# Performance work log

Hardware: AMD Instinct MI355X
Metric: run time of the kernel (lower is better)

## Reference

```python
import jax, jax.numpy as jnp
import numpy as np

LATENT = 256
C = 512            # channels == window_size
STEP = C // 2      # 256
N_SAMPLES = 32768
N_FRAMES = N_SAMPLES // STEP   # 128
IMP = 4096         # impulse samples
B, E = 4, 64
EPS = 1e-8


def unit_norm(x, axis=-1):
    return x / (jnp.linalg.norm(x, axis=axis, keepdims=True) + EPS)


def hamming(n):
    # torch.hamming_window default (periodic=True)
    return (0.54 - 0.46 * jnp.cos(2.0 * jnp.pi * jnp.arange(n) / n)).astype(jnp.float32)


def layer_norm(x, g, b):
    mu = x.mean(-1, keepdims=True)
    var = x.var(-1, keepdims=True)
    return (x - mu) / jnp.sqrt(var + 1e-5) * g + b


def mlp(x, Ws, bs, g, bt):
    # LinearOutputStack: 3 hidden (linear -> LayerNorm -> leaky_relu) + output linear
    for j in range(3):
        x = x @ Ws[j] + bs[j]
        x = layer_norm(x, g[j], bt[j])
        x = jax.nn.leaky_relu(x, 0.2)
    return x @ Ws[3] + bs[3]


def _forward(embedding, impulse, W_def, b_def,
             Ws_imp, bs_imp, g_imp, bt_imp,
             Ws_lat, bs_lat, g_lat, bt_lat,
             Ws_out, bs_out, g_out, bt_out,
             W_w, b_w, W_b, b_b, W_l, b_l):
    Bq, Eq, _ = embedding.shape
    # shape deformations: latent -> (C, n_frames), unit-normed over channel dim
    deform = (embedding @ W_def + b_def).reshape(Bq, Eq, C, N_FRAMES)
    deform = unit_norm(deform, axis=2)
    deform = deform.transpose(0, 1, 3, 2)           # (B,E,T,C)
    weights = deform @ W_w + b_w                    # (B,E,T,C)
    biases = deform @ W_b + b_b                     # (B,E,T,C)
    leak = 0.1 + jax.nn.sigmoid(deform @ W_l + b_l) * 0.98  # (B,E,T,1)

    # window the impulse: frames of size C with hop STEP
    padded = jnp.pad(impulse, ((0, 0), (0, 0), (0, STEP)))
    starts = jnp.arange(IMP // STEP) * STEP
    idx = starts[:, None] + jnp.arange(C)[None, :]
    windowed = padded[..., idx]                     # (B,E,16,C)
    norms = jnp.linalg.norm(windowed, axis=-1, keepdims=True)
    emb = mlp(windowed, Ws_imp, bs_imp, g_imp, bt_imp)
    emb = unit_norm(emb) * norms                    # (B,E,16,C)
    # pad with zeros to n_frames: adding zero == original i < n_impulse_frames guard
    emb_pad = jnp.pad(emb, ((0, 0), (0, 0), (0, N_FRAMES - emb.shape[2]), (0, 0)))

    ham = hamming(C)

    xs = (weights.transpose(2, 0, 1, 3),
          biases.transpose(2, 0, 1, 3),
          leak.transpose(2, 0, 1, 3),
          emb_pad.transpose(2, 0, 1, 3))

    def step(h, x):
        w, b, lk, e = x
        h = h + e
        cn = jnp.linalg.norm(h, axis=-1, keepdims=True)
        h = h * w + b
        h = unit_norm(h) * cn
        ol = mlp(h, Ws_lat, bs_lat, g_lat, bt_lat)
        ol = unit_norm(ol) * (cn * lk)
        on = jnp.linalg.norm(ol, axis=-1, keepdims=True)
        h = h - ol
        h = unit_norm(h) * (cn - on)
        of = mlp(ol, Ws_out, bs_out, g_out, bt_out)
        of = of * ham
        of = unit_norm(of) * on
        return h, of

    h0 = jnp.zeros((Bq, Eq, C), dtype=embedding.dtype)
    _, frames = jax.lax.scan(step, h0, xs)          # (T,B,E,C)
    frames = frames.transpose(1, 2, 0, 3)           # (B,E,T,C)

    # overlap-add at hop STEP, trim to n_samples
    L = (N_FRAMES - 1) * STEP + C
    oa_idx = jnp.arange(N_FRAMES)[:, None] * STEP + jnp.arange(C)[None, :]
    out = jnp.zeros((Bq, Eq, L), dtype=embedding.dtype)
    out = out.at[:, :, oa_idx].add(frames)
    return out[..., :N_SAMPLES]


def setup_inputs() -> dict:
    key = jax.random.key(0)
    ks = jax.random.split(key, 24)
    s = 0.02
    d = {
        'embedding': jax.random.normal(ks[0], (B, E, LATENT), jnp.float32),
        'impulse': jax.random.normal(ks[1], (B, E, IMP), jnp.float32),
        'W_def': jax.random.normal(ks[2], (LATENT, C * N_FRAMES), jnp.float32) * s,
        'b_def': jnp.zeros((C * N_FRAMES,), jnp.float32),
        'W_w': jax.random.normal(ks[3], (C, C), jnp.float32) * s,
        'b_w': jnp.zeros((C,), jnp.float32),
        'W_b': jax.random.normal(ks[4], (C, C), jnp.float32) * s,
        'b_b': jnp.zeros((C,), jnp.float32),
        'W_l': jax.random.normal(ks[5], (C, 1), jnp.float32) * s,
        'b_l': jnp.zeros((1,), jnp.float32),
    }
    for name, k in (('imp', ks[6]), ('lat', ks[7]), ('out', ks[8])):
        d['Ws_' + name] = jax.random.normal(k, (4, C, C), jnp.float32) * s
        d['bs_' + name] = jnp.zeros((4, C), jnp.float32)
        d['g_' + name] = jnp.ones((3, C), jnp.float32)
        d['bt_' + name] = jnp.zeros((3, C), jnp.float32)
    return d


def reference(embedding, impulse, W_def, b_def,
              Ws_imp, bs_imp, g_imp, bt_imp,
              Ws_lat, bs_lat, g_lat, bt_lat,
              Ws_out, bs_out, g_out, bt_out,
              W_w, b_w, W_b, b_b, W_l, b_l):
    return _forward(embedding, impulse, W_def, b_def,
                    Ws_imp, bs_imp, g_imp, bt_imp,
                    Ws_lat, bs_lat, g_lat, bt_lat,
                    Ws_out, bs_out, g_out, bt_out,
                    W_w, b_w, W_b, b_b, W_l, b_l)
```

## Files before the change

### kernel.cpp

```cpp
#include <hip/hip_runtime.h>
#include <math.h>

#define NB 4
#define NE 64
#define BE 256
#define LAT 256
#define NC 512
#define NT 128
#define NDEF 65536
#define NIMP 4096
#define NF 16
#define EPSN 1e-8f
#define SPB 4
#define NSCAN 64

typedef unsigned short ushort8 __attribute__((ext_vector_type(8)));
typedef short short8v __attribute__((ext_vector_type(8)));
typedef float f32x4 __attribute__((ext_vector_type(4)));

__device__ __forceinline__ unsigned short f2bf(float f) {
  const unsigned u = __float_as_uint(f);
  return (unsigned short)((u + 0x7FFFu + ((u >> 16) & 1u)) >> 16);
}

__device__ __forceinline__ void bar_nodrain() {
  asm volatile("s_waitcnt lgkmcnt(0)" ::: "memory");
  __builtin_amdgcn_s_barrier();
  __builtin_amdgcn_sched_barrier(0);
}

template <int NR>
__device__ __forceinline__ void blk_reduce1(const float* v, float* out,
                                            float* red) {
  const int tid = threadIdx.x, wave = tid >> 6, lane = tid & 63;
  float s[NR];
#pragma unroll
  for (int i = 0; i < NR; ++i) s[i] = v[i];
#pragma unroll
  for (int off = 32; off; off >>= 1) {
#pragma unroll
    for (int i = 0; i < NR; ++i) s[i] += __shfl_down(s[i], off);
  }
  if (lane == 0) {
#pragma unroll
    for (int i = 0; i < NR; ++i) red[wave * NR + i] = s[i];
  }
  bar_nodrain();
#pragma unroll
  for (int i = 0; i < NR; ++i) {
    float a = 0.f;
#pragma unroll
    for (int w = 0; w < 8; ++w) a += red[w * NR + i];
    out[i] = a;
  }
}

__global__ __launch_bounds__(64) void k_cvt(const float* __restrict__ W,
                                            unsigned short* __restrict__ Wmf) {
  const int lane = threadIdx.x;
  const int gg = blockIdx.x;
  const int p = gg & 3;
  const int kt = (gg >> 2) & 15;
  const int wv = (gg >> 6) & 7;
  const int layer = gg >> 9;
  const int col = wv * 64 + p * 16 + (lane & 15);
  const int k0 = kt * 32 + (lane >> 4) * 8;
  ushort8 o;
#pragma unroll
  for (int j = 0; j < 8; ++j)
    o[j] = f2bf(W[((size_t)layer * NC + k0 + j) * NC + col]);
  *reinterpret_cast<ushort8*>(Wmf + ((size_t)gg * 64 + lane) * 8) = o;
}

__global__ __launch_bounds__(256) void k_deform(
    const float* __restrict__ emb, const float* __restrict__ Wd,
    const float* __restrict__ bd, float* __restrict__ deform) {
  __shared__ float As[32][LAT];
  const int tid = threadIdx.x;
  const int c = blockIdx.x * 256 + tid;
  const int m0 = blockIdx.y * 32;
  for (int i = 0; i < 32; ++i) As[i][tid] = emb[(m0 + i) * LAT + tid];
  __syncthreads();
  float acc[32];
#pragma unroll
  for (int i = 0; i < 32; ++i) acc[i] = 0.f;
  for (int k = 0; k < LAT; k += 4) {
    const float w0 = Wd[(size_t)(k + 0) * NDEF + c];
    const float w1 = Wd[(size_t)(k + 1) * NDEF + c];
    const float w2 = Wd[(size_t)(k + 2) * NDEF + c];
    const float w3 = Wd[(size_t)(k + 3) * NDEF + c];
#pragma unroll
    for (int i = 0; i < 32; ++i) {
      const float4 a = *reinterpret_cast<const float4*>(&As[i][k]);
      acc[i] = fmaf(a.x, w0, acc[i]);
      acc[i] = fmaf(a.y, w1, acc[i]);
      acc[i] = fmaf(a.z, w2, acc[i]);
      acc[i] = fmaf(a.w, w3, acc[i]);
    }
  }
  const float bv = bd[c];
  for (int i = 0; i < 32; ++i)
    deform[(size_t)(m0 + i) * NDEF + c] = acc[i] + bv;
}

__global__ __launch_bounds__(512) void k_wb(
    const float* __restrict__ deform, const float* __restrict__ Ww,
    const float* __restrict__ bw, const float* __restrict__ Wb,
    const float* __restrict__ bb, const float* __restrict__ Wl,
    const float* __restrict__ bl, float* __restrict__ weights,
    float* __restrict__ biases, float* __restrict__ leak) {
  __shared__ float xs[16][NC];
  __shared__ float rno[16], lks[16];
  const int tid = threadIdx.x;
  const int wave = tid >> 6, lane = tid & 63;
  const int be = blockIdx.x >> 3;
  const int t0 = (blockIdx.x & 7) * 16;
  const float* dbase = deform + (size_t)be * NDEF;
  for (int i = 0; i < 16; ++i)
    xs[i][tid] = dbase[(size_t)tid * NT + t0 + i];
  __syncthreads();
  for (int f = wave; f < 16; f += 8) {
    float s = 0.f;
#pragma unroll
    for (int j = 0; j < 8; ++j) {
      const float v = xs[f][lane + 64 * j];
      s = fmaf(v, v, s);
    }
#pragma unroll
    for (int off = 32; off; off >>= 1) s += __shfl_down(s, off);
    if (lane == 0) rno[f] = sqrtf(s);
  }
  __syncthreads();
#pragma unroll
  for (int i = 0; i < 16; ++i) xs[i][tid] = xs[i][tid] / (rno[i] + EPSN);
  __syncthreads();
  for (int f = wave; f < 16; f += 8) {
    float s = 0.f;
#pragma unroll
    for (int j = 0; j < 8; ++j)
      s = fmaf(xs[f][lane + 64 * j], Wl[lane + 64 * j], s);
#pragma unroll
    for (int off = 32; off; off >>= 1) s += __shfl_down(s, off);
    if (lane == 0) lks[f] = s;
  }
  __syncthreads();
  if (tid < 16) {
    const float v = lks[tid] + bl[0];
    leak[(size_t)be * NT + t0 + tid] = 0.1f + 0.98f / (1.f + expf(-v));
  }
  float accw[16], accb[16];
#pragma unroll
  for (int i = 0; i < 16; ++i) { accw[i] = 0.f; accb[i] = 0.f; }
  for (int k = 0; k < NC; k += 2) {
    const float w0 = Ww[(size_t)k * NC + tid];
    const float w1 = Ww[(size_t)(k + 1) * NC + tid];
    const float v0 = Wb[(size_t)k * NC + tid];
    const float v1 = Wb[(size_t)(k + 1) * NC + tid];
#pragma unroll
    for (int i = 0; i < 16; ++i) {
      const float2 a = *reinterpret_cast<const float2*>(&xs[i][k]);
      accw[i] = fmaf(a.x, w0, accw[i]);
      accw[i] = fmaf(a.y, w1, accw[i]);
      accb[i] = fmaf(a.x, v0, accb[i]);
      accb[i] = fmaf(a.y, v1, accb[i]);
    }
  }
  const float bwv = bw[tid], bbv = bb[tid];
  for (int i = 0; i < 16; ++i) {
    const size_t o = ((size_t)be * NT + t0 + i) * NC + tid;
    weights[o] = accw[i] + bwv;
    biases[o] = accb[i] + bbv;
  }
}

__device__ __forceinline__ void tile_gemm16(const float (*xs)[NC],
                                            const float* __restrict__ W,
                                            int tid, float acc[16]) {
#pragma unroll
  for (int i = 0; i < 16; ++i) acc[i] = 0.f;
  for (int k = 0; k < NC; k += 4) {
    const float w0 = W[(size_t)(k + 0) * NC + tid];
    const float w1 = W[(size_t)(k + 1) * NC + tid];
    const float w2 = W[(size_t)(k + 2) * NC + tid];
    const float w3 = W[(size_t)(k + 3) * NC + tid];
#pragma unroll
    for (int i = 0; i < 16; ++i) {
      const float4 a = *reinterpret_cast<const float4*>(&xs[i][k]);
      acc[i] = fmaf(a.x, w0, acc[i]);
      acc[i] = fmaf(a.y, w1, acc[i]);
      acc[i] = fmaf(a.z, w2, acc[i]);
      acc[i] = fmaf(a.w, w3, acc[i]);
    }
  }
}

__device__ __forceinline__ void ln_leaky16(float (*xs)[NC],
                                           const float* __restrict__ g,
                                           const float* __restrict__ bt,
                                           int layer, int tid, float* mu_s,
                                           float* rs_s) {
  const int wave = tid >> 6, lane = tid & 63;
  for (int f = wave; f < 16; f += 8) {
    float s = 0.f, s2 = 0.f;
#pragma unroll
    for (int j = 0; j < 8; ++j) {
      const float v = xs[f][lane + 64 * j];
      s += v;
      s2 = fmaf(v, v, s2);
    }
#pragma unroll
    for (int off = 32; off; off >>= 1) {
      s += __shfl_down(s, off);
      s2 += __shfl_down(s2, off);
    }
    if (lane == 0) {
      const float mu = s * (1.f / NC);
      mu_s[f] = mu;
      rs_s[f] = rsqrtf(s2 * (1.f / NC) - mu * mu + 1e-5f);
    }
  }
  __syncthreads();
  const float gv = g[layer * NC + tid], btv = bt[layer * NC + tid];
#pragma unroll
  for (int i = 0; i < 16; ++i) {
    const float y = (xs[i][tid] - mu_s[i]) * rs_s[i] * gv + btv;
    xs[i][tid] = y > 0.f ? y : 0.2f * y;
  }
  __syncthreads();
}

__global__ __launch_bounds__(512) void k_imp(
    const float* __restrict__ impulse, const float* __restrict__ Ws,
    const float* __restrict__ bs, const float* __restrict__ g,
    const float* __restrict__ bt, float* __restrict__ embo) {
  __shared__ float xs[16][NC];
  __shared__ float wno[16], mu_s[16], rs_s[16], ono[16];
  const int tid = threadIdx.x;
  const int wave = tid >> 6, lane = tid & 63;
  const int be = blockIdx.x;
  const float* ib = impulse + (size_t)be * NIMP;
  for (int f = 0; f < 16; ++f) {
    const int s = f * 256 + tid;
    xs[f][tid] = (s < NIMP) ? ib[s] : 0.f;
  }
  __syncthreads();
  for (int f = wave; f < 16; f += 8) {
    float s = 0.f;
#pragma unroll
    for (int j = 0; j < 8; ++j) {
      const float v = xs[f][lane + 64 * j];
      s = fmaf(v, v, s);
    }
#pragma unroll
    for (int off = 32; off; off >>= 1) s += __shfl_down(s, off);
    if (lane == 0) wno[f] = sqrtf(s);
  }
  __syncthreads();
  float acc[16];
  for (int layer = 0; layer < 4; ++layer) {
    tile_gemm16(xs, Ws + (size_t)layer * NC * NC, tid, acc);
    __syncthreads();
    const float bv = bs[layer * NC + tid];
#pragma unroll
    for (int i = 0; i < 16; ++i) xs[i][tid] = acc[i] + bv;
    __syncthreads();
    if (layer < 3) ln_leaky16(xs, g, bt, layer, tid, mu_s, rs_s);
  }
  for (int f = wave; f < 16; f += 8) {
    float s = 0.f;
#pragma unroll
    for (int j = 0; j < 8; ++j) {
      const float v = xs[f][lane + 64 * j];
      s = fmaf(v, v, s);
    }
#pragma unroll
    for (int off = 32; off; off >>= 1) s += __shfl_down(s, off);
    if (lane == 0) ono[f] = sqrtf(s);
  }
  __syncthreads();
  for (int f = 0; f < 16; ++f)
    embo[((size_t)be * NF + f) * NC + tid] =
        xs[f][tid] / (ono[f] + EPSN) * wno[f];
}

__global__ __launch_bounds__(512) void k_scan(
    const float* __restrict__ weights, const float* __restrict__ biases,
    const float* __restrict__ leak, const float* __restrict__ embw,
    const unsigned short* __restrict__ Wmf, const float* __restrict__ bs,
    const float* __restrict__ g, const float* __restrict__ bt,
    float* __restrict__ olb, float* __restrict__ onb) {
  __shared__ __align__(16) unsigned short A_lds[16 * NC];
  __shared__ __align__(16) unsigned short B_lds[8][4][2048];
  __shared__ float ol_lds[SPB][NC];
  __shared__ float redA[64];
  __shared__ float redB[32];
  __shared__ float st1[8][SPB], st2[8][SPB];
  __shared__ float lk_lds[SPB][NT];

  const int tid = threadIdx.x;
  const int wave = tid >> 6, lane = tid & 63;
  const int seq0 = blockIdx.x * SPB;

  {
    const int r = tid >> 7, tt = tid & 127;
    lk_lds[r][tt] = leak[(size_t)(seq0 + r) * NT + tt];
  }
  {
    unsigned* z = (unsigned*)(A_lds + SPB * NC);
    for (int i = tid; i < (16 - SPB) * NC / 2; i += 512) z[i] = 0u;
  }

  const int arow = lane & 15;
  const int kgrp = lane >> 4;
  const int abase = arow * (NC * 2);
  const int axor = (arow & 7) << 4;
  const int akoff = kgrp * 16;
  const bool crow = (kgrp == 0);

  float bsv[4][4], gv[3][4], btv[3][4];
#pragma unroll
  for (int p = 0; p < 4; ++p) {
    const int cp = wave * 64 + p * 16 + (lane & 15);
#pragma unroll
    for (int l = 0; l < 4; ++l) bsv[l][p] = bs[l * NC + cp];
#pragma unroll
    for (int l = 0; l < 3; ++l) {
      gv[l][p] = g[l * NC + cp];
      btv[l][p] = bt[l * NC + cp];
    }
  }
  const unsigned short* wfrag = Wmf + (size_t)wave * 32768 + lane * 8;

  auto issue_chunk = [&](int cc) {
    const int layer = cc >> 4, kt = cc & 15, slot = cc & 3;
#pragma unroll
    for (int p = 0; p < 4; ++p) {
      __builtin_amdgcn_global_load_lds(
          (const unsigned int*)(wfrag + (size_t)layer * 262144 +
                                (kt * 4 + p) * 512),
          (unsigned int*)&B_lds[wave][slot][p * 512], 16, 0, 0);
    }
  };

  float wpre[SPB], bpre[SPB], epre[SPB];
#pragma unroll
  for (int r = 0; r < SPB; ++r) {
    const size_t o = ((size_t)(seq0 + r) * NT) * NC + tid;
    wpre[r] = weights[o];
    bpre[r] = biases[o];
    epre[r] = embw[((size_t)(seq0 + r) * NF) * NC + tid];
  }

  __syncthreads();

  issue_chunk(0);
  issue_chunk(1);
  issue_chunk(2);

  float h[SPB], cn[SPB];
#pragma unroll
  for (int r = 0; r < SPB; ++r) { h[r] = 0.f; cn[r] = 0.f; }

#pragma unroll 1
  for (int t = 0; t < NT; ++t) {
    float hw[SPB];
    if (t < NF) {
#pragma unroll
      for (int r = 0; r < SPB; ++r) h[r] += epre[r];
      if (t + 1 < NF) {
#pragma unroll
        for (int r = 0; r < SPB; ++r)
          epre[r] = embw[((size_t)(seq0 + r) * NF + t + 1) * NC + tid];
      }
      float v8[8], s8[8];
#pragma unroll
      for (int r = 0; r < SPB; ++r) {
        hw[r] = fmaf(h[r], wpre[r], bpre[r]);
        v8[r] = h[r] * h[r];
        v8[SPB + r] = hw[r] * hw[r];
      }
      blk_reduce1<8>(v8, s8, redA);
#pragma unroll
      for (int r = 0; r < SPB; ++r) {
        cn[r] = sqrtf(s8[r]);
        h[r] = hw[r] * (cn[r] / (sqrtf(s8[SPB + r]) + EPSN));
      }
    } else {
      float v4[SPB], s4[SPB];
#pragma unroll
      for (int r = 0; r < SPB; ++r) {
        hw[r] = fmaf(h[r], wpre[r], bpre[r]);
        v4[r] = hw[r] * hw[r];
      }
      blk_reduce1<SPB>(v4, s4, redA);
#pragma unroll
      for (int r = 0; r < SPB; ++r)
        h[r] = hw[r] * (cn[r] / (sqrtf(s4[r]) + EPSN));
    }
    if (t + 1 < NT) {
#pragma unroll
      for (int r = 0; r < SPB; ++r) {
        const size_t o = ((size_t)(seq0 + r) * NT + t + 1) * NC + tid;
        wpre[r] = weights[o];
        bpre[r] = biases[o];
      }
    }
    {
      char* ab = (char*)A_lds;
#pragma unroll
      for (int r = 0; r < SPB; ++r)
        *(unsigned short*)(ab + r * 1024 + ((tid * 2) ^ ((r & 7) << 4))) =
            f2bf(h[r]);
    }
    bar_nodrain();

#pragma unroll 1
    for (int layer = 0; layer < 4; ++layer) {
      f32x4 acc[4];
#pragma unroll
      for (int p = 0; p < 4; ++p) acc[p] = (f32x4){0.f, 0.f, 0.f, 0.f};
#pragma unroll
      for (int kt = 0; kt < 16; ++kt) {
        asm volatile("s_waitcnt vmcnt(8)" ::: "memory");
        const short8v a = *(const short8v*)((const char*)A_lds + abase +
                                            (((kt * 64) + akoff) ^ axor));
        const int slot = kt & 3;
#pragma unroll
        for (int p = 0; p < 4; ++p) {
          const short8v b =
              *(const short8v*)((const char*)&B_lds[wave][slot][0] + p * 1024 +
                                lane * 16);
          acc[p] =
              __builtin_amdgcn_mfma_f32_16x16x32_bf16(a, b, acc[p], 0, 0, 0);
        }
        issue_chunk((layer * 16 + kt + 3) & 63);
      }

      if (layer < 3) {
        float s1[SPB], s2[SPB];
#pragma unroll
        for (int q = 0; q < SPB; ++q) { s1[q] = 0.f; s2[q] = 0.f; }
#pragma unroll
        for (int p = 0; p < 4; ++p) {
#pragma unroll
          for (int q = 0; q < SPB; ++q) {
            const float y = acc[p][q] + bsv[layer][p];
            acc[p][q] = y;
            s1[q] += y;
            s2[q] = fmaf(y, y, s2[q]);
          }
        }
#pragma unroll
        for (int off = 1; off < 16; off <<= 1) {
#pragma unroll
          for (int q = 0; q < SPB; ++q) {
            s1[q] += __shfl_xor(s1[q], off);
            s2[q] += __shfl_xor(s2[q], off);
          }
        }
        if (lane == 0) {
#pragma unroll
          for (int q = 0; q < SPB; ++q) {
            st1[wave][q] = s1[q];
            st2[wave][q] = s2[q];
          }
        }
        bar_nodrain();
        float mu[SPB], rs[SPB];
#pragma unroll
        for (int q = 0; q < SPB; ++q) {
          float a1 = 0.f, a2 = 0.f;
#pragma unroll
          for (int w = 0; w < 8; ++w) {
            a1 += st1[w][q];
            a2 += st2[w][q];
          }
          mu[q] = a1 * (1.f / NC);
          rs[q] = rsqrtf(a2 * (1.f / NC) - mu[q] * mu[q] + 1e-5f);
        }
        if (crow) {
          char* ab = (char*)A_lds;
#pragma unroll
          for (int q = 0; q < SPB; ++q) {
#pragma unroll
            for (int p = 0; p < 4; ++p) {
              float y = (acc[p][q] - mu[q]) * rs[q] * gv[layer][p] +
                        btv[layer][p];
              y = y > 0.f ? y : 0.2f * y;
              const int cp = wave * 64 + p * 16 + (lane & 15);
              *(unsigned short*)(ab + q * 1024 +
                                 ((cp * 2) ^ ((q & 7) << 4))) = f2bf(y);
            }
          }
        }
        bar_nodrain();
      } else {
        float s2[SPB];
#pragma unroll
        for (int q = 0; q < SPB; ++q) s2[q] = 0.f;
#pragma unroll
        for (int p = 0; p < 4; ++p) {
#pragma unroll
          for (int q = 0; q < SPB; ++q) {
            const float y = acc[p][q] + bsv[3][p];
            acc[p][q] = y;
            s2[q] = fmaf(y, y, s2[q]);
          }
        }
#pragma unroll
        for (int off = 1; off < 16; off <<= 1) {
#pragma unroll
          for (int q = 0; q < SPB; ++q) s2[q] += __shfl_xor(s2[q], off);
        }
        if (lane == 0) {
#pragma unroll
          for (int q = 0; q < SPB; ++q) st2[wave][q] = s2[q];
        }
        if (crow) {
#pragma unroll
          for (int q = 0; q < SPB; ++q) {
#pragma unroll
            for (int p = 0; p < 4; ++p)
              ol_lds[q][wave * 64 + p * 16 + (lane & 15)] = acc[p][q];
          }
        }
        bar_nodrain();
        float sc[SPB], on[SPB];
#pragma unroll
        for (int r = 0; r < SPB; ++r) {
          float a2 = 0.f;
#pragma unroll
          for (int w = 0; w < 8; ++w) a2 += st2[w][r];
          const float no = sqrtf(a2);
          sc[r] = cn[r] * lk_lds[r][t] / (no + EPSN);
          on[r] = no * sc[r];
        }
        if (tid < SPB) onb[(size_t)(seq0 + tid) * NT + t] = on[tid];
        float v4[SPB], s4[SPB];
#pragma unroll
        for (int r = 0; r < SPB; ++r) {
          const float olv = ol_lds[r][tid] * sc[r];
          olb[((size_t)(seq0 + r) * NT + t) * NC + tid] = olv;
          h[r] -= olv;
          v4[r] = h[r] * h[r];
        }
        blk_reduce1<SPB>(v4, s4, redB);
#pragma unroll
        for (int r = 0; r < SPB; ++r) {
          h[r] *= (cn[r] - on[r]) / (sqrtf(s4[r]) + EPSN);
          cn[r] = fabsf(cn[r] - on[r]);
        }
      }
    }
  }
}

__global__ __launch_bounds__(512) void k_out(
    const float* __restrict__ olb, const float* __restrict__ onb,
    const unsigned short* __restrict__ Wmf, const float* __restrict__ bs,
    const float* __restrict__ g, const float* __restrict__ bt,
    float* __restrict__ ofb) {
  __shared__ __align__(16) unsigned short A_lds[16 * NC];
  __shared__ float st1[8][16], st2[8][16];
  __shared__ float on_l[16];
  const int tid = threadIdx.x;
  const int wave = tid >> 6, lane = tid & 63;
  const int m0 = blockIdx.x * 16;
  const int arow = lane & 15;
  const int kgrp = lane >> 4;
  const int r0 = kgrp * 4;
  const int abase = arow * (NC * 2);
  const int axor = (arow & 7) << 4;
  const int akoff = kgrp * 16;

  float bsv[4][4], gv[3][4], btv[3][4], hamv[4];
#pragma unroll
  for (int p = 0; p < 4; ++p) {
    const int cp = wave * 64 + p * 16 + (lane & 15);
#pragma unroll
    for (int l = 0; l < 4; ++l) bsv[l][p] = bs[l * NC + cp];
#pragma unroll
    for (int l = 0; l < 3; ++l) {
      gv[l][p] = g[l * NC + cp];
      btv[l][p] = bt[l * NC + cp];
    }
    hamv[p] =
        0.54f - 0.46f * cosf(6.283185307179586f * (float)cp / (float)NC);
  }
  if (tid < 16) on_l[tid] = onb[m0 + tid];
  {
    char* ab = (char*)A_lds;
    for (int i = 0; i < 16; ++i) {
      const float v = olb[(size_t)(m0 + i) * NC + tid];
      *(unsigned short*)(ab + i * 1024 + ((tid * 2) ^ ((i & 7) << 4))) =
          f2bf(v);
    }
  }
  __syncthreads();

  const unsigned short* wfrag = Wmf + (size_t)wave * 32768 + lane * 8;

#pragma unroll 1
  for (int layer = 0; layer < 4; ++layer) {
    f32x4 acc[4];
#pragma unroll
    for (int p = 0; p < 4; ++p) acc[p] = (f32x4){0.f, 0.f, 0.f, 0.f};
#pragma unroll
    for (int kt = 0; kt < 16; ++kt) {
      const short8v a = *(const short8v*)((const char*)A_lds + abase +
                                          (((kt * 64) + akoff) ^ axor));
#pragma unroll
      for (int p = 0; p < 4; ++p) {
        const short8v b = *(const short8v*)(wfrag + (size_t)layer * 262144 +
                                            (kt * 4 + p) * 512);
        acc[p] = __builtin_amdgcn_mfma_f32_16x16x32_bf16(a, b, acc[p], 0, 0, 0);
      }
    }
    if (layer < 3) {
      float s1[4], s2[4];
#pragma unroll
      for (int q = 0; q < 4; ++q) { s1[q] = 0.f; s2[q] = 0.f; }
#pragma unroll
      for (int p = 0; p < 4; ++p) {
#pragma unroll
        for (int q = 0; q < 4; ++q) {
          const float y = acc[p][q] + bsv[layer][p];
          acc[p][q] = y;
          s1[q] += y;
          s2[q] = fmaf(y, y, s2[q]);
        }
      }
#pragma unroll
      for (int off = 1; off < 16; off <<= 1) {
#pragma unroll
        for (int q = 0; q < 4; ++q) {
          s1[q] += __shfl_xor(s1[q], off);
          s2[q] += __shfl_xor(s2[q], off);
        }
      }
      if ((lane & 15) == 0) {
#pragma unroll
        for (int q = 0; q < 4; ++q) {
          st1[wave][r0 + q] = s1[q];
          st2[wave][r0 + q] = s2[q];
        }
      }
      __syncthreads();
      char* ab = (char*)A_lds;
#pragma unroll
      for (int q = 0; q < 4; ++q) {
        const int row = r0 + q;
        float a1 = 0.f, a2 = 0.f;
#pragma unroll
        for (int w = 0; w < 8; ++w) {
          a1 += st1[w][row];
          a2 += st2[w][row];
        }
        const float mu = a1 * (1.f / NC);
        const float rs = rsqrtf(a2 * (1.f / NC) - mu * mu + 1e-5f);
#pragma unroll
        for (int p = 0; p < 4; ++p) {
          float y = (acc[p][q] - mu) * rs * gv[layer][p] + btv[layer][p];
          y = y > 0.f ? y : 0.2f * y;
          const int cp = wave * 64 + p * 16 + (lane & 15);
          *(unsigned short*)(ab + row * 1024 +
                             ((cp * 2) ^ ((row & 7) << 4))) = f2bf(y);
        }
      }
      __syncthreads();
    } else {
      float s2[4];
#pragma unroll
      for (int q = 0; q < 4; ++q) s2[q] = 0.f;
#pragma unroll
      for (int p = 0; p < 4; ++p) {
#pragma unroll
        for (int q = 0; q < 4; ++q) {
          float y = (acc[p][q] + bsv[3][p]) * hamv[p];
          acc[p][q] = y;
          s2[q] = fmaf(y, y, s2[q]);
        }
      }
#pragma unroll
      for (int off = 1; off < 16; off <<= 1) {
#pragma unroll
        for (int q = 0; q < 4; ++q) s2[q] += __shfl_xor(s2[q], off);
      }
      if ((lane & 15) == 0) {
#pragma unroll
        for (int q = 0; q < 4; ++q) st2[wave][r0 + q] = s2[q];
      }
      __syncthreads();
#pragma unroll
      for (int q = 0; q < 4; ++q) {
        const int row = r0 + q;
        float a2 = 0.f;
#pragma unroll
        for (int w = 0; w < 8; ++w) a2 += st2[w][row];
        const float inv = on_l[row] / (sqrtf(a2) + EPSN);
#pragma unroll
        for (int p = 0; p < 4; ++p) {
          const int cp = wave * 64 + p * 16 + (lane & 15);
          ofb[(size_t)(m0 + row) * NC + cp] = acc[p][q] * inv;
        }
      }
    }
  }
}

__global__ __launch_bounds__(256) void k_oa(const float* __restrict__ ofb,
                                            float* __restrict__ out) {
  const int idx = blockIdx.x * 256 + threadIdx.x;
  if (idx >= BE * 32768) return;
  const int be = idx >> 15;
  const int s = idx & 32767;
  const int t1 = s >> 8;
  float v = ofb[((size_t)be * NT + t1) * NC + (s - (t1 << 8))];
  if (t1 >= 1)
    v += ofb[((size_t)be * NT + (t1 - 1)) * NC + (s - ((t1 - 1) << 8))];
  out[idx] = v;
}

extern "C" void kernel_launch(void* const* d_in, const int* in_sizes, int n_in,
                              void* d_out, int out_size, void* d_ws,
                              size_t ws_size, hipStream_t stream) {
  const float* embedding = (const float*)d_in[0];
  const float* impulse = (const float*)d_in[1];
  const float* W_def = (const float*)d_in[2];
  const float* b_def = (const float*)d_in[3];
  const float* W_w = (const float*)d_in[4];
  const float* b_w = (const float*)d_in[5];
  const float* W_b = (const float*)d_in[6];
  const float* b_b = (const float*)d_in[7];
  const float* W_l = (const float*)d_in[8];
  const float* b_l = (const float*)d_in[9];
  const float* Ws_imp = (const float*)d_in[10];
  const float* bs_imp = (const float*)d_in[11];
  const float* g_imp = (const float*)d_in[12];
  const float* bt_imp = (const float*)d_in[13];
  const float* Ws_lat = (const float*)d_in[14];
  const float* bs_lat = (const float*)d_in[15];
  const float* g_lat = (const float*)d_in[16];
  const float* bt_lat = (const float*)d_in[17];
  const float* Ws_out = (const float*)d_in[18];
  const float* bs_out = (const float*)d_in[19];
  const float* g_out = (const float*)d_in[20];
  const float* bt_out = (const float*)d_in[21];
  float* out = (float*)d_out;

  float* ws = (float*)d_ws;
  float* deform = ws;
  float* weights = deform + 16777216;
  float* biases = weights + 16777216;
  float* leakb = biases + 16777216;
  float* embw = leakb + 32768;
  float* onb = embw + 2097152;
  unsigned short* wmf = (unsigned short*)(onb + 32768);
  unsigned short* wmf_out = wmf + 1048576;
  float* olb = deform;
  float* ofb = weights;

  k_cvt<<<2048, 64, 0, stream>>>(Ws_lat, wmf);
  k_cvt<<<2048, 64, 0, stream>>>(Ws_out, wmf_out);
  k_deform<<<dim3(256, 8), 256, 0, stream>>>(embedding, W_def, b_def, deform);
  k_wb<<<2048, 512, 0, stream>>>(deform, W_w, b_w, W_b, b_b, W_l, b_l,
                                 weights, biases, leakb);
  k_imp<<<256, 512, 0, stream>>>(impulse, Ws_imp, bs_imp, g_imp, bt_imp, embw);
  k_scan<<<NSCAN, 512, 0, stream>>>(weights, biases, leakb, embw, wmf, bs_lat,
                                    g_lat, bt_lat, olb, onb);
  k_out<<<2048, 512, 0, stream>>>(olb, onb, wmf_out, bs_out, g_out, bt_out,
                                  ofb);
  k_oa<<<32768, 256, 0, stream>>>(ofb, out);
}
```

Before: 5.002 ms.

## Use bf16 MFMA for weights/biases projection in k_wb

Replaces the scalar FP32 FMA GEMM that computes weights and biases from the normalized deform tile with bf16 MFMA 16x16x32 instructions. The normalized activations are written to a swizzled bf16 LDS buffer, and W_w/W_b are pre-converted into MFMA fragment layout by extra k_cvt launches. This cuts ALU work on a large GEMM (4*64*128 rows x 512 x 1024). The cost is reduced precision from bf16 inputs and extra LDS use.

```diff
diff --git a/kernel.cpp b/kernel.cpp
--- a/kernel.cpp
+++ b/kernel.cpp
@@ -104,12 +104,13 @@
 }
 
 __global__ __launch_bounds__(512) void k_wb(
-    const float* __restrict__ deform, const float* __restrict__ Ww,
-    const float* __restrict__ bw, const float* __restrict__ Wb,
-    const float* __restrict__ bb, const float* __restrict__ Wl,
-    const float* __restrict__ bl, float* __restrict__ weights,
-    float* __restrict__ biases, float* __restrict__ leak) {
+    const float* __restrict__ deform, const unsigned short* __restrict__ Wmf2,
+    const float* __restrict__ bw, const float* __restrict__ bb,
+    const float* __restrict__ Wl, const float* __restrict__ bl,
+    float* __restrict__ weights, float* __restrict__ biases,
+    float* __restrict__ leak) {
   __shared__ float xs[16][NC];
+  __shared__ __align__(16) unsigned short A_lds[16 * NC];
   __shared__ float rno[16], lks[16];
   const int tid = threadIdx.x;
   const int wave = tid >> 6, lane = tid & 63;
@@ -131,8 +132,16 @@
     if (lane == 0) rno[f] = sqrtf(s);
   }
   __syncthreads();
-#pragma unroll
-  for (int i = 0; i < 16; ++i) xs[i][tid] = xs[i][tid] / (rno[i] + EPSN);
+  {
+    char* ab = (char*)A_lds;
+#pragma unroll
+    for (int i = 0; i < 16; ++i) {
+      const float xv = xs[i][tid] / (rno[i] + EPSN);
+      xs[i][tid] = xv;
+      *(unsigned short*)(ab + i * 1024 + ((tid * 2) ^ ((i & 7) << 4))) =
+          f2bf(xv);
+    }
+  }
   __syncthreads();
   for (int f = wave; f < 16; f += 8) {
     float s = 0.f;
@@ -148,28 +157,49 @@
     const float v = lks[tid] + bl[0];
     leak[(size_t)be * NT + t0 + tid] = 0.1f + 0.98f / (1.f + expf(-v));
   }
-  float accw[16], accb[16];
-#pragma unroll
-  for (int i = 0; i < 16; ++i) { accw[i] = 0.f; accb[i] = 0.f; }
-  for (int k = 0; k < NC; k += 2) {
-    const float w0 = Ww[(size_t)k * NC + tid];
-    const float w1 = Ww[(size_t)(k + 1) * NC + tid];
-    const float v0 = Wb[(size_t)k * NC + tid];
-    const float v1 = Wb[(size_t)(k + 1) * NC + tid];
-#pragma unroll
-    for (int i = 0; i < 16; ++i) {
-      const float2 a = *reinterpret_cast<const float2*>(&xs[i][k]);
-      accw[i] = fmaf(a.x, w0, accw[i]);
-      accw[i] = fmaf(a.y, w1, accw[i]);
-      accb[i] = fmaf(a.x, v0, accb[i]);
-      accb[i] = fmaf(a.y, v1, accb[i]);
-    }
-  }
-  const float bwv = bw[tid], bbv = bb[tid];
-  for (int i = 0; i < 16; ++i) {
-    const size_t o = ((size_t)be * NT + t0 + i) * NC + tid;
-    weights[o] = accw[i] + bwv;
-    biases[o] = accb[i] + bbv;
+  const int arow = lane & 15;
+  const int kgrp = lane >> 4;
+  const int r0 = kgrp * 4;
+  const int abase = arow * (NC * 2);
+  const int axor = (arow & 7) << 4;
+  const int akoff = kgrp * 16;
+  float bwv[4], bbv[4];
+#pragma unroll
+  for (int p = 0; p < 4; ++p) {
+    const int cp = wave * 64 + p * 16 + (lane & 15);
+    bwv[p] = bw[cp];
+    bbv[p] = bb[cp];
+  }
+  const unsigned short* wfrag = Wmf2 + (size_t)wave * 32768 + lane * 8;
+  f32x4 accw[4], accb[4];
+#pragma unroll
+  for (int p = 0; p < 4; ++p) {
+    accw[p] = (f32x4){0.f, 0.f, 0.f, 0.f};
+    accb[p] = (f32x4){0.f, 0.f, 0.f, 0.f};
+  }
+#pragma unroll
+  for (int kt = 0; kt < 16; ++kt) {
+    const short8v a = *(const short8v*)((const char*)A_lds + abase +
+                                        (((kt * 64) + akoff) ^ axor));
+#pragma unroll
+    for (int p = 0; p < 4; ++p) {
+      const short8v b0 = *(const short8v*)(wfrag + (kt * 4 + p) * 512);
+      accw[p] = __builtin_amdgcn_mfma_f32_16x16x32_bf16(a, b0, accw[p], 0, 0, 0);
+      const short8v b1 =
+          *(const short8v*)(wfrag + (size_t)262144 + (kt * 4 + p) * 512);
+      accb[p] = __builtin_amdgcn_mfma_f32_16x16x32_bf16(a, b1, accb[p], 0, 0, 0);
+    }
+  }
+#pragma unroll
+  for (int q = 0; q < 4; ++q) {
+    const int row = r0 + q;
+#pragma unroll
+    for (int p = 0; p < 4; ++p) {
+      const int cp = wave * 64 + p * 16 + (lane & 15);
+      const size_t o = ((size_t)be * NT + t0 + row) * NC + cp;
+      weights[o] = accw[p][q] + bwv[p];
+      biases[o] = accb[p][q] + bbv[p];
+    }
   }
 }
 
@@ -757,13 +787,16 @@
   float* onb = embw + 2097152;
   unsigned short* wmf = (unsigned short*)(onb + 32768);
   unsigned short* wmf_out = wmf + 1048576;
+  unsigned short* wmf_wb = wmf_out + 1048576;
   float* olb = deform;
   float* ofb = weights;
 
   k_cvt<<<2048, 64, 0, stream>>>(Ws_lat, wmf);
   k_cvt<<<2048, 64, 0, stream>>>(Ws_out, wmf_out);
+  k_cvt<<<512, 64, 0, stream>>>(W_w, wmf_wb);
+  k_cvt<<<512, 64, 0, stream>>>(W_b, wmf_wb + 262144);
   k_deform<<<dim3(256, 8), 256, 0, stream>>>(embedding, W_def, b_def, deform);
-  k_wb<<<2048, 512, 0, stream>>>(deform, W_w, b_w, W_b, b_b, W_l, b_l,
+  k_wb<<<2048, 512, 0, stream>>>(deform, wmf_wb, b_w, b_b, W_l, b_l,
                                  weights, biases, leakb);
   k_imp<<<256, 512, 0, stream>>>(impulse, Ws_imp, bs_imp, g_imp, bt_imp, embw);
   k_scan<<<NSCAN, 512, 0, stream>>>(weights, biases, leakb, embw, wmf, bs_lat,
```

New measurement: 4.474 ms. 1.12x faster.
